# Optimization experiments

Measured on AMD Instinct MI355X. Metric: run time of the kernel, lower is better.

## Reference

```python
import jax, jax.numpy as jnp
import numpy as np

D_MODEL = 1024
N_HEADS = 16
HEAD_DIM = D_MODEL // N_HEADS
B, L = 2, 2048


def setup_inputs() -> dict:
    key = jax.random.key(0)
    ks = jax.random.split(key, 11)
    s = 1.0 / np.sqrt(D_MODEL)
    inp = {
        'query': jax.random.normal(ks[0], (B, L, D_MODEL), dtype=jnp.float32),
        'key': jax.random.normal(ks[1], (B, L, D_MODEL), dtype=jnp.float32),
        'value': jax.random.normal(ks[2], (B, L, D_MODEL), dtype=jnp.float32),
        'Wq_w': jax.random.normal(ks[3], (D_MODEL, D_MODEL), dtype=jnp.float32) * s,
        'Wq_b': jnp.zeros((D_MODEL,), dtype=jnp.float32),
        'Wk_w': jax.random.normal(ks[4], (D_MODEL, D_MODEL), dtype=jnp.float32) * s,
        'Wk_b': jnp.zeros((D_MODEL,), dtype=jnp.float32),
        'Wv_w': jax.random.normal(ks[5], (D_MODEL, D_MODEL), dtype=jnp.float32) * s,
        'Wv_b': jnp.zeros((D_MODEL,), dtype=jnp.float32),
        'Wo_w': jax.random.normal(ks[6], (D_MODEL, D_MODEL), dtype=jnp.float32) * s,
        'Wo_b': jnp.zeros((D_MODEL,), dtype=jnp.float32),
    }
    return inp


def reference(query, key, value, Wq_w, Wq_b, Wk_w, Wk_b, Wv_w, Wv_b, Wo_w, Wo_b):
    b = query.shape[0]
    # torch Linear: y = x @ W^T + b
    Q = query @ Wq_w.T + Wq_b
    K = key @ Wk_w.T + Wk_b
    V = value @ Wv_w.T + Wv_b
    # [B, L, D] -> [B, H, L, hd]
    def split_heads(x):
        return x.reshape(b, -1, N_HEADS, HEAD_DIM).transpose(0, 2, 1, 3)
    Qh, Kh, Vh = split_heads(Q), split_heads(K), split_heads(V)
    scale = 1.0 / jnp.sqrt(jnp.float32(HEAD_DIM))
    # energy: [B, H, Lq, Lk]
    energy = jnp.einsum('bhqd,bhkd->bhqk', Qh, Kh) * scale
    # NOTE: original code applies softmax over dim=1 (the HEADS axis) — faithful reproduction
    attn = jax.nn.softmax(energy, axis=1)
    out = jnp.einsum('bhqk,bhkd->bhqd', attn, Vh)  # [B, H, Lq, hd]
    out = out.transpose(0, 2, 1, 3).reshape(b, -1, D_MODEL)
    return out @ Wo_w.T + Wo_b
```

## Files before the change

### kernel.cpp

```cpp
#include <hip/hip_runtime.h>
#include <hip/hip_bf16.h>
#include <hip/hip_fp16.h>

#define DM 1024
#define NH 16
#define HD 64
#define LL 2048

typedef __attribute__((ext_vector_type(8))) short bf16x8;
typedef __attribute__((ext_vector_type(4))) float f32x4;

#define MFMA16(a,b,c) __builtin_amdgcn_mfma_f32_16x16x32_bf16((a),(b),(c),0,0,0)

#define GL16(g, l) __builtin_amdgcn_global_load_lds( \
    (const __attribute__((address_space(1))) unsigned int*)(g), \
    (__attribute__((address_space(3))) unsigned int*)(l), 16, 0, 0)

__device__ __forceinline__ ushort f2bf(float f) {
  union { float f; unsigned int u; } v; v.f = f;
  unsigned int u = v.u + 0x7fffu + ((v.u >> 16) & 1u);
  return (ushort)(u >> 16);
}

__global__ __launch_bounds__(256) void cvt6(const float* __restrict__ s0, ushort* __restrict__ d0, int n0,
                                            const float* __restrict__ s1, ushort* __restrict__ d1, int n1,
                                            const float* __restrict__ s2, ushort* __restrict__ d2, int n2,
                                            const float* __restrict__ s3, ushort* __restrict__ d3, int n3,
                                            const float* __restrict__ s4, ushort* __restrict__ d4, int n4,
                                            const float* __restrict__ s5, ushort* __restrict__ d5, int n5) {
  int i = (blockIdx.x * 256 + threadIdx.x) * 4;
  const float* s; ushort* d;
  if (i < n0) { s = s0; d = d0; }
  else if ((i -= n0) < n1) { s = s1; d = d1; }
  else if ((i -= n1) < n2) { s = s2; d = d2; }
  else if ((i -= n2) < n3) { s = s3; d = d3; }
  else if ((i -= n3) < n4) { s = s4; d = d4; }
  else if ((i -= n4) < n5) { s = s5; d = d5; }
  else return;
  float4 v = *(const float4*)(s + i);
  union { ushort u[4]; unsigned long long ll; } o;
  o.u[0] = f2bf(v.x); o.u[1] = f2bf(v.y); o.u[2] = f2bf(v.z); o.u[3] = f2bf(v.w);
  *(unsigned long long*)(d + i) = o.ll;
}

__global__ __launch_bounds__(256) void gemm_qkv(const ushort* __restrict__ qA, const ushort* __restrict__ qW,
                                                const float* __restrict__ qb, ushort* __restrict__ qO,
                                                const ushort* __restrict__ kA, const ushort* __restrict__ kW,
                                                const float* __restrict__ kb, ushort* __restrict__ kO,
                                                const ushort* __restrict__ vA, const ushort* __restrict__ vW,
                                                const float* __restrict__ vb, ushort* __restrict__ vO) {
  __shared__ ushort lA[2][128][64];
  __shared__ ushort lB[2][128][64];
  const int z = blockIdx.z;
  const ushort* Ab; const ushort* Wb; const float* bias; ushort* outp;
  float alpha; bool trans;
  if (z == 0)      { Ab = qA; Wb = qW; bias = qb; outp = qO; alpha = 0.125f; trans = false; }
  else if (z == 1) { Ab = kA; Wb = kW; bias = kb; outp = kO; alpha = 1.0f;   trans = false; }
  else             { Ab = vA; Wb = vW; bias = vb; outp = vO; alpha = 1.0f;   trans = true;  }

  const int m0 = blockIdx.x * 128, n0 = blockIdx.y * 128;
  const int t = threadIdx.x;
  const int w = t >> 6, lane = t & 63, lr = lane & 15, lg = lane >> 4;
  const int wm = (w >> 1) * 64, wn = (w & 1) * 64;
  const int lrow8 = lane >> 3;
  const int scol = ((lane & 7) ^ lrow8) * 8;

  f32x4 acc[4][4];
  #pragma unroll
  for (int i = 0; i < 4; ++i)
    #pragma unroll
    for (int j = 0; j < 4; ++j) acc[i][j] = (f32x4){0.f, 0.f, 0.f, 0.f};

  #pragma unroll
  for (int c = 0; c < 4; ++c) {
    GL16(Ab + (m0 + w * 32 + c * 8 + lrow8) * DM + scol, &lA[0][w * 32 + c * 8][0]);
    GL16(Wb + (n0 + w * 32 + c * 8 + lrow8) * DM + scol, &lB[0][w * 32 + c * 8][0]);
  }
  __syncthreads();

  int cur = 0;
  for (int k0 = 0; k0 < DM; k0 += 64) {
    if (k0 + 64 < DM) {
      #pragma unroll
      for (int c = 0; c < 4; ++c) {
        GL16(Ab + (m0 + w * 32 + c * 8 + lrow8) * DM + k0 + 64 + scol, &lA[cur ^ 1][w * 32 + c * 8][0]);
        GL16(Wb + (n0 + w * 32 + c * 8 + lrow8) * DM + k0 + 64 + scol, &lB[cur ^ 1][w * 32 + c * 8][0]);
      }
    }
    #pragma unroll
    for (int ks = 0; ks < 2; ++ks) {
      bf16x8 aF[4], bF[4];
      #pragma unroll
      for (int i = 0; i < 4; ++i)
        aF[i] = *(const bf16x8*)&lA[cur][wm + i * 16 + lr][(((ks * 4 + lg) ^ (lr & 7)) * 8)];
      #pragma unroll
      for (int j = 0; j < 4; ++j)
        bF[j] = *(const bf16x8*)&lB[cur][wn + j * 16 + lr][(((ks * 4 + lg) ^ (lr & 7)) * 8)];
      #pragma unroll
      for (int i = 0; i < 4; ++i)
        #pragma unroll
        for (int j = 0; j < 4; ++j)
          acc[i][j] = MFMA16(aF[i], bF[j], acc[i][j]);
    }
    __syncthreads();
    cur ^= 1;
  }

  #pragma unroll
  for (int i = 0; i < 4; ++i)
    #pragma unroll
    for (int j = 0; j < 4; ++j)
      #pragma unroll
      for (int r = 0; r < 4; ++r) {
        int m = m0 + wm + i * 16 + lg * 4 + r;
        int n = n0 + wn + j * 16 + lr;
        float v = (acc[i][j][r] + bias[n]) * alpha;
        int b = m >> 11, q = m & 2047, h = n >> 6, d = n & 63;
        if (!trans)
          outp[((b * NH + h) * LL + q) * HD + d] = f2bf(v);
        else
          outp[((b * NH + h) * HD + d) * LL + q] = f2bf(v);
      }
}

__global__ __launch_bounds__(256) void gemm_out(const ushort* __restrict__ Ab,
                                                const ushort* __restrict__ Wb,
                                                const float* __restrict__ bias,
                                                float* __restrict__ outf) {
  __shared__ ushort lA[2][64][64];
  __shared__ ushort lB[2][128][64];
  const int m0 = blockIdx.x * 64, n0 = blockIdx.y * 128;
  const int t = threadIdx.x;
  const int w = t >> 6, lane = t & 63, lr = lane & 15, lg = lane >> 4;
  const int wm = (w >> 1) * 32, wn = (w & 1) * 64;
  const int lrow8 = lane >> 3;
  const int scol = ((lane & 7) ^ lrow8) * 8;

  f32x4 acc[2][4];
  #pragma unroll
  for (int i = 0; i < 2; ++i)
    #pragma unroll
    for (int j = 0; j < 4; ++j) acc[i][j] = (f32x4){0.f, 0.f, 0.f, 0.f};

  #pragma unroll
  for (int c = 0; c < 2; ++c)
    GL16(Ab + (m0 + w * 16 + c * 8 + lrow8) * DM + scol, &lA[0][w * 16 + c * 8][0]);
  #pragma unroll
  for (int c = 0; c < 4; ++c)
    GL16(Wb + (n0 + w * 32 + c * 8 + lrow8) * DM + scol, &lB[0][w * 32 + c * 8][0]);
  __syncthreads();

  int cur = 0;
  for (int k0 = 0; k0 < DM; k0 += 64) {
    if (k0 + 64 < DM) {
      #pragma unroll
      for (int c = 0; c < 2; ++c)
        GL16(Ab + (m0 + w * 16 + c * 8 + lrow8) * DM + k0 + 64 + scol, &lA[cur ^ 1][w * 16 + c * 8][0]);
      #pragma unroll
      for (int c = 0; c < 4; ++c)
        GL16(Wb + (n0 + w * 32 + c * 8 + lrow8) * DM + k0 + 64 + scol, &lB[cur ^ 1][w * 32 + c * 8][0]);
    }
    #pragma unroll
    for (int ks = 0; ks < 2; ++ks) {
      bf16x8 aF[2], bF[4];
      #pragma unroll
      for (int i = 0; i < 2; ++i)
        aF[i] = *(const bf16x8*)&lA[cur][wm + i * 16 + lr][(((ks * 4 + lg) ^ (lr & 7)) * 8)];
      #pragma unroll
      for (int j = 0; j < 4; ++j)
        bF[j] = *(const bf16x8*)&lB[cur][wn + j * 16 + lr][(((ks * 4 + lg) ^ (lr & 7)) * 8)];
      #pragma unroll
      for (int i = 0; i < 2; ++i)
        #pragma unroll
        for (int j = 0; j < 4; ++j)
          acc[i][j] = MFMA16(aF[i], bF[j], acc[i][j]);
    }
    __syncthreads();
    cur ^= 1;
  }

  #pragma unroll
  for (int i = 0; i < 2; ++i)
    #pragma unroll
    for (int j = 0; j < 4; ++j)
      #pragma unroll
      for (int r = 0; r < 4; ++r) {
        int m = m0 + wm + i * 16 + lg * 4 + r;
        int n = n0 + wn + j * 16 + lr;
        outf[m * DM + n] = acc[i][j][r] + bias[n];
      }
}

__global__ __launch_bounds__(256) void pass_a_m(const ushort* __restrict__ Qh,
                                                const ushort* __restrict__ Kh,
                                                __half* __restrict__ rdenH) {
  __shared__ ushort lQ[2][128][64];
  __shared__ ushort lK[2][128][64];
  const int b = blockIdx.z, q0 = blockIdx.y * 128, k0 = blockIdx.x * 128;
  const int t = threadIdx.x, w = t >> 6, lane = t & 63, lr = lane & 15, lg = lane >> 4;
  const int lrow8 = lane >> 3;
  const int scol = ((lane & 7) ^ lrow8) * 8;

  f32x4 acc[2][8];
  #pragma unroll
  for (int i = 0; i < 2; ++i)
    #pragma unroll
    for (int j = 0; j < 8; ++j) acc[i][j] = (f32x4){0.f, 0.f, 0.f, 0.f};

  #pragma unroll
  for (int c = 0; c < 4; ++c) {
    GL16(Qh + ((b * NH) * LL + q0 + w * 32 + c * 8 + lrow8) * HD + scol, &lQ[0][w * 32 + c * 8][0]);
    GL16(Kh + ((b * NH) * LL + k0 + w * 32 + c * 8 + lrow8) * HD + scol, &lK[0][w * 32 + c * 8][0]);
  }
  __syncthreads();

  int cur = 0;
  for (int h = 0; h < NH; ++h) {
    if (h + 1 < NH) {
      #pragma unroll
      for (int c = 0; c < 4; ++c) {
        GL16(Qh + ((b * NH + h + 1) * LL + q0 + w * 32 + c * 8 + lrow8) * HD + scol, &lQ[cur ^ 1][w * 32 + c * 8][0]);
        GL16(Kh + ((b * NH + h + 1) * LL + k0 + w * 32 + c * 8 + lrow8) * HD + scol, &lK[cur ^ 1][w * 32 + c * 8][0]);
      }
    }
    #pragma unroll
    for (int i = 0; i < 2; ++i) {
      int qrow = w * 32 + i * 16 + lr;
      bf16x8 a0 = *(const bf16x8*)&lQ[cur][qrow][((lg ^ (lr & 7)) * 8)];
      bf16x8 a1 = *(const bf16x8*)&lQ[cur][qrow][(((4 + lg) ^ (lr & 7)) * 8)];
      #pragma unroll
      for (int j = 0; j < 8; ++j) {
        int krow = j * 16 + lr;
        bf16x8 b0 = *(const bf16x8*)&lK[cur][krow][((lg ^ (lr & 7)) * 8)];
        bf16x8 b1 = *(const bf16x8*)&lK[cur][krow][(((4 + lg) ^ (lr & 7)) * 8)];
        f32x4 e = {0.f, 0.f, 0.f, 0.f};
        e = MFMA16(b0, a0, e);
        e = MFMA16(b1, a1, e);
        #pragma unroll
        for (int r = 0; r < 4; ++r) acc[i][j][r] += __expf(e[r]);
      }
    }
    __syncthreads();
    cur ^= 1;
  }

  #pragma unroll
  for (int i = 0; i < 2; ++i)
    #pragma unroll
    for (int j = 0; j < 8; ++j) {
      int q = q0 + w * 32 + i * 16 + lr;
      int k = k0 + j * 16 + lg * 4;
      union { __half2 h2[2]; uint2 u; } pk;
      pk.h2[0] = __floats2half2_rn(__builtin_amdgcn_rcpf(acc[i][j][0]),
                                   __builtin_amdgcn_rcpf(acc[i][j][1]));
      pk.h2[1] = __floats2half2_rn(__builtin_amdgcn_rcpf(acc[i][j][2]),
                                   __builtin_amdgcn_rcpf(acc[i][j][3]));
      *(uint2*)&rdenH[(size_t)(b * LL + q) * LL + k] = pk.u;
    }
}

#define PB_BODY(PH)                                                              \
  {                                                                              \
    const int T = tt + PH;                                                       \
    const int k0 = T * 64;                                                       \
    uint2 rdN[4];                                                                \
    if (T + 1 < 32) {                                                            \
      GL16(Kh + (bh * LL + k0 + 64 + w * 8 + lrow8) * HD + scol,                 \
           &lK[PH ^ 1][w * 8][0]);                                               \
      GL16(Vt + (bh * HD + w * 8 + lrow8) * LL + k0 + 64 + scol,                 \
           &lV[PH ^ 1][w * 8][0]);                                               \
      _Pragma("unroll")                                                          \
      for (int j = 0; j < 4; ++j)                                                \
        rdN[j] = *(const uint2*)(rrow + k0 + 64 + j * 16 + lg * 4);              \
    }                                                                            \
    __builtin_amdgcn_s_setprio(1);                                               \
    if (T > 0) {                                                                 \
      bf16x8 aP0 = *(const bf16x8*)&U.p[w][lr][lg * 8];                          \
      bf16x8 aP1 = *(const bf16x8*)&U.p[w][lr][32 + lg * 8];                     \
      _Pragma("unroll")                                                          \
      for (int j = 0; j < 4; ++j) {                                              \
        accO[j] = MFMA16(aP0, vF0[j], accO[j]);                                  \
        accO[j] = MFMA16(aP1, vF1[j], accO[j]);                                  \
      }                                                                          \
    }                                                                            \
    f32x4 e[4];                                                                  \
    _Pragma("unroll")                                                            \
    for (int j = 0; j < 4; ++j) {                                                \
      int krow = j * 16 + lr;                                                    \
      bf16x8 kf0 = *(const bf16x8*)&lK[PH][krow][((lg ^ (lr & 7)) * 8)];         \
      bf16x8 kf1 = *(const bf16x8*)&lK[PH][krow][(((4 + lg) ^ (lr & 7)) * 8)];   \
      e[j] = (f32x4){0.f, 0.f, 0.f, 0.f};                                        \
      e[j] = MFMA16(kf0, aQ0, e[j]);                                             \
      e[j] = MFMA16(kf1, aQ1, e[j]);                                             \
    }                                                                            \
    __builtin_amdgcn_s_setprio(0);                                               \
    _Pragma("unroll")                                                            \
    for (int j = 0; j < 4; ++j) {                                                \
      int vrow = j * 16 + lr;                                                    \
      vF0[j] = *(const bf16x8*)&lV[PH][vrow][((lg ^ (lr & 7)) * 8)];             \
      vF1[j] = *(const bf16x8*)&lV[PH][vrow][(((4 + lg) ^ (lr & 7)) * 8)];       \
    }                                                                            \
    _Pragma("unroll")                                                            \
    for (int j = 0; j < 4; ++j) {                                                \
      float2 f0 = __half22float2(*reinterpret_cast<const __half2*>(&rdC[j].x));  \
      float2 f1 = __half22float2(*reinterpret_cast<const __half2*>(&rdC[j].y));  \
      union { __hip_bfloat162 b2[2]; uint2 u; } pk;                              \
      pk.b2[0] = __float22bfloat162_rn(make_float2(__expf(e[j][0]) * f0.x,       \
                                                   __expf(e[j][1]) * f0.y));     \
      pk.b2[1] = __float22bfloat162_rn(make_float2(__expf(e[j][2]) * f1.x,       \
                                                   __expf(e[j][3]) * f1.y));     \
      *(uint2*)&U.p[w][lr][j * 16 + lg * 4] = pk.u;                              \
    }                                                                            \
    if (T + 1 < 32) {                                                            \
      _Pragma("unroll")                                                          \
      for (int j = 0; j < 4; ++j) rdC[j] = rdN[j];                               \
    }                                                                            \
    __syncthreads();                                                             \
  }

__global__ __launch_bounds__(512, 4) void pass_b_m(const ushort* __restrict__ Qh,
                                                   const ushort* __restrict__ Kh,
                                                   const ushort* __restrict__ Vt,
                                                   const __half* __restrict__ rdenH,
                                                   ushort* __restrict__ AO) {
  __shared__ union UQP { ushort q[128][64]; ushort p[8][16][72]; } U;
  __shared__ ushort lK[2][64][64];
  __shared__ ushort lV[2][64][64];
  const int q0 = blockIdx.x * 128, h = blockIdx.y, b = blockIdx.z;
  const int t = threadIdx.x, w = t >> 6, lane = t & 63, lr = lane & 15, lg = lane >> 4;
  const int lrow8 = lane >> 3;
  const int scol = ((lane & 7) ^ lrow8) * 8;
  const int bh = b * NH + h;

  #pragma unroll
  for (int u = 0; u < 2; ++u) {
    int c = u * 512 + t;
    int row = c >> 3, col = (c & 7) * 8;
    *(bf16x8*)&U.q[row][col] = *(const bf16x8*)&Qh[(bh * LL + q0 + row) * HD + col];
  }
  GL16(Kh + (bh * LL + w * 8 + lrow8) * HD + scol, &lK[0][w * 8][0]);
  GL16(Vt + (bh * HD + w * 8 + lrow8) * LL + scol, &lV[0][w * 8][0]);
  const int qg = q0 + w * 16 + lr;
  const __half* rrow = rdenH + (size_t)(b * LL + qg) * LL;
  uint2 rdC[4];
  #pragma unroll
  for (int j = 0; j < 4; ++j) rdC[j] = *(const uint2*)(rrow + j * 16 + lg * 4);
  __syncthreads();

  bf16x8 aQ0 = *(const bf16x8*)&U.q[w * 16 + lr][lg * 8];
  bf16x8 aQ1 = *(const bf16x8*)&U.q[w * 16 + lr][32 + lg * 8];
  __syncthreads();

  f32x4 accO[4];
  #pragma unroll
  for (int j = 0; j < 4; ++j) accO[j] = (f32x4){0.f, 0.f, 0.f, 0.f};
  bf16x8 vF0[4], vF1[4];

  for (int tt = 0; tt < 32; tt += 2) {
    PB_BODY(0)
    PB_BODY(1)
  }

  {
    bf16x8 aP0 = *(const bf16x8*)&U.p[w][lr][lg * 8];
    bf16x8 aP1 = *(const bf16x8*)&U.p[w][lr][32 + lg * 8];
    #pragma unroll
    for (int j = 0; j < 4; ++j) {
      accO[j] = MFMA16(aP0, vF0[j], accO[j]);
      accO[j] = MFMA16(aP1, vF1[j], accO[j]);
    }
  }

  #pragma unroll
  for (int j = 0; j < 4; ++j)
    #pragma unroll
    for (int r = 0; r < 4; ++r) {
      int q = q0 + w * 16 + lg * 4 + r;
      int d = j * 16 + lr;
      AO[(b * LL + q) * DM + h * HD + d] = f2bf(accO[j][r]);
    }
}

extern "C" void kernel_launch(void* const* d_in, const int* in_sizes, int n_in,
                              void* d_out, int out_size, void* d_ws, size_t ws_size,
                              hipStream_t stream) {
  const float* query = (const float*)d_in[0];
  const float* key   = (const float*)d_in[1];
  const float* value = (const float*)d_in[2];
  const float* Wq_w  = (const float*)d_in[3];
  const float* Wq_b  = (const float*)d_in[4];
  const float* Wk_w  = (const float*)d_in[5];
  const float* Wk_b  = (const float*)d_in[6];
  const float* Wv_w  = (const float*)d_in[7];
  const float* Wv_b  = (const float*)d_in[8];
  const float* Wo_w  = (const float*)d_in[9];
  const float* Wo_b  = (const float*)d_in[10];

  char* ws = (char*)d_ws;
  char* dob = (char*)d_out;
  ushort* Qh  = (ushort*)(ws);
  ushort* Kh  = (ushort*)(ws + (8u  << 20));
  ushort* Vt  = (ushort*)(ws + (16u << 20));
  ushort* AO  = (ushort*)(ws + (24u << 20));
  ushort* qbf = (ushort*)(ws + (32u << 20));
  ushort* kbf = (ushort*)(ws + (40u << 20));
  ushort* Wob = (ushort*)(ws + (32u << 20));
  ushort* vbf = (ushort*)(dob);
  ushort* Wqb = (ushort*)(dob + (8u  << 20));
  ushort* Wkb = (ushort*)(dob + (10u << 20));
  ushort* Wvb = (ushort*)(dob + (12u << 20));
  __half* rdn = (__half*)d_out;

  const int NA = 2 * LL * DM;
  const int NW = DM * DM;

  cvt6<<<(3 * NA + 3 * NW) / 1024, 256, 0, stream>>>(
      query, qbf, NA, key, kbf, NA, value, vbf, NA,
      Wq_w, Wqb, NW, Wk_w, Wkb, NW, Wv_w, Wvb, NW);

  gemm_qkv<<<dim3(32, 8, 3), 256, 0, stream>>>(qbf, Wqb, Wq_b, Qh,
                                               kbf, Wkb, Wk_b, Kh,
                                               vbf, Wvb, Wv_b, Vt);

  cvt6<<<NW / 1024, 256, 0, stream>>>(Wo_w, Wob, NW,
                                      nullptr, nullptr, 0, nullptr, nullptr, 0,
                                      nullptr, nullptr, 0, nullptr, nullptr, 0,
                                      nullptr, nullptr, 0);

  pass_a_m<<<dim3(16, 16, 2), 256, 0, stream>>>(Qh, Kh, rdn);
  pass_b_m<<<dim3(16, NH, 2), 512, 0, stream>>>(Qh, Kh, Vt, rdn, AO);

  gemm_out<<<dim3(64, 8), 256, 0, stream>>>(AO, Wob, Wo_b, (float*)d_out);
}
```

Before: 195.2 us.

## Triple-buffer K/V in attention pass and enlarge output GEMM tile

The attention pass B now keeps three LDS buffers for K and V and three register sets for reciprocal denominators, prefetching two tiles ahead. Its full __syncthreads is replaced by a partial vmcnt wait plus a raw s_barrier, so the in-flight loads can overlap the next iteration. The output projection GEMM moves from 64x128 to 128x128 tiles, halving the grid and doubling per-wave accumulators for more data reuse. In exchange, LDS and register pressure rise, and the output GEMM has fewer blocks to spread across CUs.

```diff
diff --git a/kernel.cpp b/kernel.cpp
--- a/kernel.cpp
+++ b/kernel.cpp
@@ -127,50 +127,48 @@
                                                 const ushort* __restrict__ Wb,
                                                 const float* __restrict__ bias,
                                                 float* __restrict__ outf) {
-  __shared__ ushort lA[2][64][64];
+  __shared__ ushort lA[2][128][64];
   __shared__ ushort lB[2][128][64];
-  const int m0 = blockIdx.x * 64, n0 = blockIdx.y * 128;
+  const int m0 = blockIdx.x * 128, n0 = blockIdx.y * 128;
   const int t = threadIdx.x;
   const int w = t >> 6, lane = t & 63, lr = lane & 15, lg = lane >> 4;
-  const int wm = (w >> 1) * 32, wn = (w & 1) * 64;
+  const int wm = (w >> 1) * 64, wn = (w & 1) * 64;
   const int lrow8 = lane >> 3;
   const int scol = ((lane & 7) ^ lrow8) * 8;
 
-  f32x4 acc[2][4];
-  #pragma unroll
-  for (int i = 0; i < 2; ++i)
+  f32x4 acc[4][4];
+  #pragma unroll
+  for (int i = 0; i < 4; ++i)
     #pragma unroll
     for (int j = 0; j < 4; ++j) acc[i][j] = (f32x4){0.f, 0.f, 0.f, 0.f};
 
   #pragma unroll
-  for (int c = 0; c < 2; ++c)
-    GL16(Ab + (m0 + w * 16 + c * 8 + lrow8) * DM + scol, &lA[0][w * 16 + c * 8][0]);
-  #pragma unroll
-  for (int c = 0; c < 4; ++c)
+  for (int c = 0; c < 4; ++c) {
+    GL16(Ab + (m0 + w * 32 + c * 8 + lrow8) * DM + scol, &lA[0][w * 32 + c * 8][0]);
     GL16(Wb + (n0 + w * 32 + c * 8 + lrow8) * DM + scol, &lB[0][w * 32 + c * 8][0]);
+  }
   __syncthreads();
 
   int cur = 0;
   for (int k0 = 0; k0 < DM; k0 += 64) {
     if (k0 + 64 < DM) {
       #pragma unroll
-      for (int c = 0; c < 2; ++c)
-        GL16(Ab + (m0 + w * 16 + c * 8 + lrow8) * DM + k0 + 64 + scol, &lA[cur ^ 1][w * 16 + c * 8][0]);
-      #pragma unroll
-      for (int c = 0; c < 4; ++c)
+      for (int c = 0; c < 4; ++c) {
+        GL16(Ab + (m0 + w * 32 + c * 8 + lrow8) * DM + k0 + 64 + scol, &lA[cur ^ 1][w * 32 + c * 8][0]);
         GL16(Wb + (n0 + w * 32 + c * 8 + lrow8) * DM + k0 + 64 + scol, &lB[cur ^ 1][w * 32 + c * 8][0]);
+      }
     }
     #pragma unroll
     for (int ks = 0; ks < 2; ++ks) {
-      bf16x8 aF[2], bF[4];
-      #pragma unroll
-      for (int i = 0; i < 2; ++i)
+      bf16x8 aF[4], bF[4];
+      #pragma unroll
+      for (int i = 0; i < 4; ++i)
         aF[i] = *(const bf16x8*)&lA[cur][wm + i * 16 + lr][(((ks * 4 + lg) ^ (lr & 7)) * 8)];
       #pragma unroll
       for (int j = 0; j < 4; ++j)
         bF[j] = *(const bf16x8*)&lB[cur][wn + j * 16 + lr][(((ks * 4 + lg) ^ (lr & 7)) * 8)];
       #pragma unroll
-      for (int i = 0; i < 2; ++i)
+      for (int i = 0; i < 4; ++i)
         #pragma unroll
         for (int j = 0; j < 4; ++j)
           acc[i][j] = MFMA16(aF[i], bF[j], acc[i][j]);
@@ -180,7 +178,7 @@
   }
 
   #pragma unroll
-  for (int i = 0; i < 2; ++i)
+  for (int i = 0; i < 4; ++i)
     #pragma unroll
     for (int j = 0; j < 4; ++j)
       #pragma unroll
@@ -259,63 +257,62 @@
     }
 }
 
-#define PB_BODY(PH)                                                              \
-  {                                                                              \
-    const int T = tt + PH;                                                       \
-    const int k0 = T * 64;                                                       \
-    uint2 rdN[4];                                                                \
-    if (T + 1 < 32) {                                                            \
-      GL16(Kh + (bh * LL + k0 + 64 + w * 8 + lrow8) * HD + scol,                 \
-           &lK[PH ^ 1][w * 8][0]);                                               \
-      GL16(Vt + (bh * HD + w * 8 + lrow8) * LL + k0 + 64 + scol,                 \
-           &lV[PH ^ 1][w * 8][0]);                                               \
-      _Pragma("unroll")                                                          \
-      for (int j = 0; j < 4; ++j)                                                \
-        rdN[j] = *(const uint2*)(rrow + k0 + 64 + j * 16 + lg * 4);              \
-    }                                                                            \
-    __builtin_amdgcn_s_setprio(1);                                               \
-    if (T > 0) {                                                                 \
-      bf16x8 aP0 = *(const bf16x8*)&U.p[w][lr][lg * 8];                          \
-      bf16x8 aP1 = *(const bf16x8*)&U.p[w][lr][32 + lg * 8];                     \
-      _Pragma("unroll")                                                          \
-      for (int j = 0; j < 4; ++j) {                                              \
-        accO[j] = MFMA16(aP0, vF0[j], accO[j]);                                  \
-        accO[j] = MFMA16(aP1, vF1[j], accO[j]);                                  \
-      }                                                                          \
-    }                                                                            \
-    f32x4 e[4];                                                                  \
-    _Pragma("unroll")                                                            \
-    for (int j = 0; j < 4; ++j) {                                                \
-      int krow = j * 16 + lr;                                                    \
-      bf16x8 kf0 = *(const bf16x8*)&lK[PH][krow][((lg ^ (lr & 7)) * 8)];         \
-      bf16x8 kf1 = *(const bf16x8*)&lK[PH][krow][(((4 + lg) ^ (lr & 7)) * 8)];   \
-      e[j] = (f32x4){0.f, 0.f, 0.f, 0.f};                                        \
-      e[j] = MFMA16(kf0, aQ0, e[j]);                                             \
-      e[j] = MFMA16(kf1, aQ1, e[j]);                                             \
-    }                                                                            \
-    __builtin_amdgcn_s_setprio(0);                                               \
-    _Pragma("unroll")                                                            \
-    for (int j = 0; j < 4; ++j) {                                                \
-      int vrow = j * 16 + lr;                                                    \
-      vF0[j] = *(const bf16x8*)&lV[PH][vrow][((lg ^ (lr & 7)) * 8)];             \
-      vF1[j] = *(const bf16x8*)&lV[PH][vrow][(((4 + lg) ^ (lr & 7)) * 8)];       \
-    }                                                                            \
-    _Pragma("unroll")                                                            \
-    for (int j = 0; j < 4; ++j) {                                                \
-      float2 f0 = __half22float2(*reinterpret_cast<const __half2*>(&rdC[j].x));  \
-      float2 f1 = __half22float2(*reinterpret_cast<const __half2*>(&rdC[j].y));  \
-      union { __hip_bfloat162 b2[2]; uint2 u; } pk;                              \
-      pk.b2[0] = __float22bfloat162_rn(make_float2(__expf(e[j][0]) * f0.x,       \
-                                                   __expf(e[j][1]) * f0.y));     \
-      pk.b2[1] = __float22bfloat162_rn(make_float2(__expf(e[j][2]) * f1.x,       \
-                                                   __expf(e[j][3]) * f1.y));     \
-      *(uint2*)&U.p[w][lr][j * 16 + lg * 4] = pk.u;                              \
-    }                                                                            \
-    if (T + 1 < 32) {                                                            \
-      _Pragma("unroll")                                                          \
-      for (int j = 0; j < 4; ++j) rdC[j] = rdN[j];                               \
-    }                                                                            \
-    __syncthreads();                                                             \
+#define PB_BODY(T, SC, SL, BR, BL)                                             \
+  {                                                                            \
+    if ((T) + 2 < 32) {                                                        \
+      GL16(Kh + (bh * LL + ((T) + 2) * 64 + w * 8 + lrow8) * HD + scol,        \
+           &lK[BL][w * 8][0]);                                                 \
+      GL16(Vt + (bh * HD + w * 8 + lrow8) * LL + ((T) + 2) * 64 + scol,        \
+           &lV[BL][w * 8][0]);                                                 \
+      _Pragma("unroll")                                                        \
+      for (int j = 0; j < 4; ++j)                                              \
+        SL[j] = *(const uint2*)(rrow + ((T) + 2) * 64 + j * 16 + lg * 4);      \
+    }                                                                          \
+    __builtin_amdgcn_s_setprio(1);                                             \
+    if ((T) > 0) {                                                             \
+      bf16x8 aP0 = *(const bf16x8*)&U.p[w][lr][lg * 8];                        \
+      bf16x8 aP1 = *(const bf16x8*)&U.p[w][lr][32 + lg * 8];                   \
+      _Pragma("unroll")                                                        \
+      for (int j = 0; j < 4; ++j) {                                            \
+        accO[j] = MFMA16(aP0, vF0[j], accO[j]);                                \
+        accO[j] = MFMA16(aP1, vF1[j], accO[j]);                                \
+      }                                                                        \
+    }                                                                          \
+    f32x4 e[4];                                                                \
+    _Pragma("unroll")                                                          \
+    for (int j = 0; j < 4; ++j) {                                              \
+      int krow = j * 16 + lr;                                                  \
+      bf16x8 kf0 = *(const bf16x8*)&lK[BR][krow][((lg ^ (lr & 7)) * 8)];       \
+      bf16x8 kf1 = *(const bf16x8*)&lK[BR][krow][(((4 + lg) ^ (lr & 7)) * 8)]; \
+      e[j] = (f32x4){0.f, 0.f, 0.f, 0.f};                                      \
+      e[j] = MFMA16(kf0, aQ0, e[j]);                                           \
+      e[j] = MFMA16(kf1, aQ1, e[j]);                                           \
+    }                                                                          \
+    __builtin_amdgcn_s_setprio(0);                                             \
+    _Pragma("unroll")                                                          \
+    for (int j = 0; j < 4; ++j) {                                              \
+      int vrow = j * 16 + lr;                                                  \
+      vF0[j] = *(const bf16x8*)&lV[BR][vrow][((lg ^ (lr & 7)) * 8)];           \
+      vF1[j] = *(const bf16x8*)&lV[BR][vrow][(((4 + lg) ^ (lr & 7)) * 8)];     \
+    }                                                                          \
+    _Pragma("unroll")                                                          \
+    for (int j = 0; j < 4; ++j) {                                              \
+      float2 f0 = __half22float2(*reinterpret_cast<const __half2*>(&SC[j].x)); \
+      float2 f1 = __half22float2(*reinterpret_cast<const __half2*>(&SC[j].y)); \
+      union { __hip_bfloat162 b2[2]; uint2 u; } pk;                            \
+      pk.b2[0] = __float22bfloat162_rn(make_float2(__expf(e[j][0]) * f0.x,     \
+                                                   __expf(e[j][1]) * f0.y));   \
+      pk.b2[1] = __float22bfloat162_rn(make_float2(__expf(e[j][2]) * f1.x,     \
+                                                   __expf(e[j][3]) * f1.y));   \
+      *(uint2*)&U.p[w][lr][j * 16 + lg * 4] = pk.u;                            \
+    }                                                                          \
+    if ((T) < 31) {                                                            \
+      if ((T) + 2 < 32) { asm volatile("s_waitcnt vmcnt(6)" ::: "memory"); }   \
+      else              { asm volatile("s_waitcnt vmcnt(0)" ::: "memory"); }   \
+      __builtin_amdgcn_sched_barrier(0);                                       \
+      __builtin_amdgcn_s_barrier();                                            \
+      __builtin_amdgcn_sched_barrier(0);                                       \
+    }                                                                          \
   }
 
 __global__ __launch_bounds__(512, 4) void pass_b_m(const ushort* __restrict__ Qh,
@@ -324,8 +321,8 @@
                                                    const __half* __restrict__ rdenH,
                                                    ushort* __restrict__ AO) {
   __shared__ union UQP { ushort q[128][64]; ushort p[8][16][72]; } U;
-  __shared__ ushort lK[2][64][64];
-  __shared__ ushort lV[2][64][64];
+  __shared__ ushort lK[3][64][64];
+  __shared__ ushort lV[3][64][64];
   const int q0 = blockIdx.x * 128, h = blockIdx.y, b = blockIdx.z;
   const int t = threadIdx.x, w = t >> 6, lane = t & 63, lr = lane & 15, lg = lane >> 4;
   const int lrow8 = lane >> 3;
@@ -340,11 +337,16 @@
   }
   GL16(Kh + (bh * LL + w * 8 + lrow8) * HD + scol, &lK[0][w * 8][0]);
   GL16(Vt + (bh * HD + w * 8 + lrow8) * LL + scol, &lV[0][w * 8][0]);
+  GL16(Kh + (bh * LL + 64 + w * 8 + lrow8) * HD + scol, &lK[1][w * 8][0]);
+  GL16(Vt + (bh * HD + w * 8 + lrow8) * LL + 64 + scol, &lV[1][w * 8][0]);
   const int qg = q0 + w * 16 + lr;
   const __half* rrow = rdenH + (size_t)(b * LL + qg) * LL;
-  uint2 rdC[4];
-  #pragma unroll
-  for (int j = 0; j < 4; ++j) rdC[j] = *(const uint2*)(rrow + j * 16 + lg * 4);
+  uint2 rA[4], rB[4], rC2[4];
+  #pragma unroll
+  for (int j = 0; j < 4; ++j) {
+    rA[j] = *(const uint2*)(rrow + j * 16 + lg * 4);
+    rB[j] = *(const uint2*)(rrow + 64 + j * 16 + lg * 4);
+  }
   __syncthreads();
 
   bf16x8 aQ0 = *(const bf16x8*)&U.q[w * 16 + lr][lg * 8];
@@ -356,10 +358,13 @@
   for (int j = 0; j < 4; ++j) accO[j] = (f32x4){0.f, 0.f, 0.f, 0.f};
   bf16x8 vF0[4], vF1[4];
 
-  for (int tt = 0; tt < 32; tt += 2) {
-    PB_BODY(0)
-    PB_BODY(1)
-  }
+  for (int tt = 0; tt < 30; tt += 3) {
+    PB_BODY(tt + 0, rA, rC2, 0, 2)
+    PB_BODY(tt + 1, rB, rA, 1, 0)
+    PB_BODY(tt + 2, rC2, rB, 2, 1)
+  }
+  PB_BODY(30, rA, rC2, 0, 2)
+  PB_BODY(31, rB, rA, 1, 0)
 
   {
     bf16x8 aP0 = *(const bf16x8*)&U.p[w][lr][lg * 8];
@@ -430,5 +435,5 @@
   pass_a_m<<<dim3(16, 16, 2), 256, 0, stream>>>(Qh, Kh, rdn);
   pass_b_m<<<dim3(16, NH, 2), 512, 0, stream>>>(Qh, Kh, Vt, rdn, AO);
 
-  gemm_out<<<dim3(64, 8), 256, 0, stream>>>(AO, Wob, Wo_b, (float*)d_out);
-}
+  gemm_out<<<dim3(32, 8), 256, 0, stream>>>(AO, Wob, Wo_b, (float*)d_out);
+}
```

Result: no change. 197.1 us (+0.9%).
